# Kernel tuning notes

Measured on AMD Instinct MI355X. Metric: run time of the kernel, lower is better.

## Reference

```python
import math
import jax, jax.numpy as jnp
import numpy as np
from jax import lax

DIM = 4096
N_STEPS = 12 * 4096  # ceil(log2(4096)) * 4096
SEED = 2024


def make_walk_params(seed, n_steps, dim):
    """Deterministic (i, j, cos, sin) schedule for one Kac random walk."""
    key = jax.random.key(seed)
    ki, kj, kt = jax.random.split(key, 3)
    i = jax.random.randint(ki, (n_steps,), 0, dim)
    j = jax.random.randint(kj, (n_steps,), 0, dim - 1)
    j = j + (j >= i).astype(j.dtype)  # ensure j != i
    theta = jax.random.uniform(kt, (n_steps,), minval=0.0, maxval=2.0 * np.pi)
    return (i.astype(jnp.int32), j.astype(jnp.int32),
            jnp.cos(theta).astype(jnp.float32), jnp.sin(theta).astype(jnp.float32))


def kac_walk(x, i_idx, j_idx, cos_t, sin_t):
    """Apply n_steps sequential 2x2 Givens rotations to columns of x [N, dim]."""
    def step(x, p):
        ii, jj, c, s = p
        xi = x[:, ii]
        xj = x[:, jj]
        x = x.at[:, ii].set(c * xi + s * xj)
        x = x.at[:, jj].set(c * xj - s * xi)
        return x, None
    x, _ = lax.scan(step, x, (i_idx, j_idx, cos_t, sin_t))
    return x


def setup_inputs() -> dict:
    key = jax.random.key(0)
    kx, kw, kb, kv = jax.random.split(key, 4)
    x = jax.random.normal(kx, (1, 512, DIM), dtype=jnp.float32)
    W = jax.random.normal(kw, (DIM, DIM), dtype=jnp.float32) / math.sqrt(DIM)
    b = jax.random.normal(kb, (DIM,), dtype=jnp.float32) * 0.01
    vec = jax.random.normal(kv, (DIM,), dtype=jnp.float32) / math.sqrt(DIM)
    i1, j1, c1, s1 = make_walk_params(SEED * 2, N_STEPS, DIM)
    i2, j2, c2, s2 = make_walk_params(SEED * 2 + 1, N_STEPS, DIM)
    return {"x": x, "W": W, "b": b, "vec": vec,
            "i1": i1, "j1": j1, "c1": c1, "s1": s1,
            "i2": i2, "j2": j2, "c2": c2, "s2": s2}


def reference(x, W, b, vec, i1, j1, c1, s1, i2, j2, c2, s2):
    # frozen base layer: y = x @ W.T + b
    y = jnp.einsum('bsd,od->bso', x, W) + b
    # Kac adapter path
    x2d = x.reshape(-1, DIM)                 # [N, dim]
    yp = kac_walk(x2d, i1, j1, c1, s1)
    yp = vec * yp                            # per-coordinate scale
    yp = kac_walk(yp, i2, j2, c2, s2)
    return y + yp.reshape(y.shape)
```

## Files before the change

kernel.cpp:

```cpp
#include <hip/hip_runtime.h>


#define DIM    4096
#define ROWS   512
#define NSTEPS 49152
#define WSTEPS 8192
#define NW2    (NSTEPS / WSTEPS)
#define NSLOT  (2 * NW2)
#define NSG    16
#define CHUNK  128
#define WVN    4
#define PWC    96
#define SLOTREC (WVN * PWC * CHUNK)
#define MAXR   96
#define PADI   4096
#define PADJ   4097
#define KT     1024
#define SPT    (WSTEPS / KT)
#define NCVW   1024
#define NCVX   128

typedef short  short8 __attribute__((ext_vector_type(8)));
typedef __bf16 bf16x8 __attribute__((ext_vector_type(8)));
typedef float  f32x4  __attribute__((ext_vector_type(4)));

__device__ inline short f2bf(float f) {
    unsigned u = __builtin_bit_cast(unsigned, f);
    u += 0x7FFFu + ((u >> 16) & 1u);
    return (short)(u >> 16);
}
__device__ inline short8 pack8(float4 a, float4 b) {
    short8 r;
    r[0] = f2bf(a.x); r[1] = f2bf(a.y); r[2] = f2bf(a.z); r[3] = f2bf(a.w);
    r[4] = f2bf(b.x); r[5] = f2bf(b.y); r[6] = f2bf(b.z); r[7] = f2bf(b.w);
    return r;
}
__device__ inline float bitf(unsigned u) { return __builtin_bit_cast(float, u); }
__device__ inline float2 ldrw(const float2* rw, int boff) {
    return *(const float2*)((const char*)rw + boff);
}
__device__ inline void strw(float2* rw, int boff, float2 v) {
    *(float2*)((char*)rw + boff) = v;
}
__device__ inline void gl16(const short* g, short* l) {
    __builtin_amdgcn_global_load_lds((const __attribute__((address_space(1))) unsigned*)g,
                                     (__attribute__((address_space(3))) unsigned*)l, 16, 0, 0);
}

__global__ __launch_bounds__(KT) void kfused(
    const int* __restrict__ i1, const int* __restrict__ j1,
    const float* __restrict__ c1, const float* __restrict__ s1,
    const int* __restrict__ i2, const int* __restrict__ j2,
    const float* __restrict__ c2, const float* __restrict__ s2,
    uint4* __restrict__ recs, int* __restrict__ nlvls, unsigned* __restrict__ lvmeta_g,
    int doconv, const float* __restrict__ W, const float* __restrict__ X,
    short* __restrict__ wb, short* __restrict__ xb) {

    if (blockIdx.x >= NSLOT) {
        if (!doconv) return;
        const int cb = blockIdx.x - NSLOT;
        const float* src; short* dst; size_t base;
        if (cb < NCVW) { src = W; dst = wb; base = (size_t)cb * 16384; }
        else           { src = X; dst = xb; base = (size_t)(cb - NCVW) * 16384; }
        const size_t o = base + (size_t)threadIdx.x * 16;
        const float4* s4 = (const float4*)(src + o);
        const float4 a0 = s4[0], a1 = s4[1], a2 = s4[2], a3 = s4[3];
        *(short8*)(dst + o)     = pack8(a0, a1);
        *(short8*)(dst + o + 8) = pack8(a2, a3);
        return;
    }

    __shared__ unsigned tbl[DIM];
    __shared__ unsigned spair[WSTEPS];
    __shared__ unsigned lvrk[WSTEPS];
    __shared__ int lcnt[MAXR * NSG];
    __shared__ unsigned lvpk[MAXR], wvbase[MAXR];
    __shared__ unsigned char serf[MAXR];
    __shared__ int nlvlsh;

    const int b    = blockIdx.x;
    const int walk = b / NW2;
    const int w    = b % NW2;
    const int t    = threadIdx.x;
    const int gb   = w * WSTEPS;
    const int sg   = t >> 6;

    const int*   I = walk ? i2 : i1;
    const int*   J = walk ? j2 : j1;
    const float* C = walk ? c2 : c1;
    const float* S = walk ? s2 : s1;

    uint4* slotp = recs + (size_t)b * SLOTREC;

    {
        const uint4 padrec = { (unsigned)(PADI * 8), 0x3F800000u, 0u, (unsigned)(PADJ * 8) };
        for (int k = t; k < SLOTREC; k += KT) slotp[k] = padrec;
    }
    for (int s = t; s < WSTEPS; s += KT)
        spair[s] = (unsigned)I[gb + s] | ((unsigned)J[gb + s] << 16);
    for (int k = t; k < DIM; k += KT) tbl[k] = 0xFFFFFFFFu;
    for (int k = t; k < MAXR * NSG; k += KT) lcnt[k] = 0;
    if (t < MAXR) serf[t] = 0;
    if (t == 0) nlvlsh = 1;
    __syncthreads();

    unsigned pmask = (1u << SPT) - 1u;
    for (int rr = 0; rr < MAXR; ++rr) {
        const unsigned rk = (unsigned)(MAXR - 1 - rr) << 13;
#pragma unroll
        for (int q = 0; q < SPT; ++q)
            if (pmask & (1u << q)) {
                const int s = q * KT + t;
                const unsigned sp = spair[s];
                const unsigned key = rk | (unsigned)s;
                atomicMin(&tbl[sp & 0xFFFFu], key);
                atomicMin(&tbl[sp >> 16], key);
            }
        __syncthreads();
#pragma unroll
        for (int q = 0; q < SPT; ++q)
            if (pmask & (1u << q)) {
                const int s = q * KT + t;
                const unsigned sp = spair[s];
                const unsigned key = rk | (unsigned)s;
                if (tbl[sp & 0xFFFFu] == key && tbl[sp >> 16] == key) {
                    const int rank = atomicAdd(&lcnt[rr * NSG + sg], 1);
                    lvrk[s] = ((unsigned)rank << 8) | (unsigned)rr;
                    pmask &= ~(1u << q);
                }
            }
        const int np = __syncthreads_count(pmask != 0);
        if (np == 0) break;
    }
#pragma unroll
    for (int q = 0; q < SPT; ++q)
        if (pmask & (1u << q)) {
            const int s = q * KT + t;
            const int rank = atomicAdd(&lcnt[(MAXR - 1) * NSG + sg], 1);
            lvrk[s] = ((unsigned)rank << 8) | (unsigned)(MAXR - 1);
        }
    __syncthreads();

    if (t < MAXR) {
        int run = 0;
        for (int g = 0; g < NSG; ++g) {
            const int v = lcnt[t * NSG + g];
            lcnt[t * NSG + g] = run;
            run += v;
        }
        const int nch = (run + 127) >> 7;
        unsigned pk = 0;
        if (run > 0 && nch <= 2) {
            serf[t] = 1;
            pk = (unsigned)nch;
        } else {
#pragma unroll
            for (int wv = 0; wv < WVN; ++wv)
                pk |= (unsigned)((nch + (WVN - 1 - wv)) >> 2) << (8 * wv);
        }
        lvpk[t] = pk;
        if (run > 0) atomicMax(&nlvlsh, t + 1);
    }
    __syncthreads();
    if (t < 64) {
        const int l = t;
        const unsigned w1 = lvpk[l];
        unsigned x1 = w1;
        for (int off = 1; off < 64; off <<= 1) {
            const unsigned v = (unsigned)__shfl_up((int)x1, off);
            if (l >= off) x1 += v;
        }
        wvbase[l] = x1 - w1;
        const unsigned seg1 = (unsigned)__shfl((int)x1, 63);
        const int l2 = 64 + (l & 31);
        const unsigned w2 = lvpk[l2];
        unsigned x2 = w2;
        for (int off = 1; off < 32; off <<= 1) {
            const unsigned v = (unsigned)__shfl_up((int)x2, off);
            if ((l & 31) >= off) x2 += v;
        }
        if (l < 32) wvbase[l2] = seg1 + x2 - w2;
    }
    __syncthreads();
    if (t < MAXR - 1) {
        if (serf[t] && serf[t + 1]) lvpk[t] |= 0x80000000u;
    }
    __syncthreads();
    if (t == 0) nlvls[b] = nlvlsh;
    if (t < MAXR) lvmeta_g[b * MAXR + t] = lvpk[t];

#pragma unroll
    for (int q = 0; q < SPT; ++q) {
        const int s = q * KT + t;
        const unsigned v = lvrk[s];
        const int lvl  = (int)(v & 0xFFu);
        const int rank = (int)(v >> 8) + lcnt[lvl * NSG + sg];
        const int cl   = rank >> 7;
        const int pos  = rank & 127;
        int wv2, wc2;
        if (serf[lvl]) { wv2 = 0; wc2 = cl; }
        else           { wv2 = cl & (WVN - 1); wc2 = cl >> 2; }
        const int pch = (int)((wvbase[lvl] >> (8 * wv2)) & 0xFFu) + wc2;
        if (pch < PWC) {
            const unsigned sp = spair[s];
            const int g = gb + s;
            uint4 r;
            r.x = (sp & 0xFFFFu) * 8u;
            r.y = __builtin_bit_cast(unsigned, C[g]);
            r.z = __builtin_bit_cast(unsigned, S[g]);
            r.w = (sp >> 16) * 8u;
            slotp[((size_t)wv2 * PWC + pch) * CHUNK + pos] = r;
        }
    }
}

__global__ __launch_bounds__(256) void kgemm_bf(const short* __restrict__ Xb, const short* __restrict__ Wb,
                                                const float* __restrict__ bias, float* __restrict__ out,
                                                float* __restrict__ parts, int nks) {
    __shared__ short As[128 * 64];
    __shared__ short Bs[128 * 64];
    const int bid  = blockIdx.x;
    const int ks   = bid % nks;
    const int tile = bid / nks;
    const int bm   = (tile >> 5) * 128;
    const int bn   = (tile & 31) * 128;
    const int tid  = threadIdx.x;
    const int lane = tid & 63;
    const int wv   = tid >> 6;
    const int wr   = (wv >> 1) * 64;
    const int wc   = (wv & 1) * 64;
    const int fr   = lane & 15;
    const int ke   = (lane >> 4) * 8;

    f32x4 acc[4][4];
#pragma unroll
    for (int m = 0; m < 4; ++m)
#pragma unroll
        for (int n = 0; n < 4; ++n) acc[m][n] = (f32x4){0.f, 0.f, 0.f, 0.f};

    const int lrow = lane >> 3;
    const int scol = (((lane & 7) ^ (lrow & 7)) << 3);
    const short* gx = Xb + (size_t)(bm + wv * 32 + lrow) * DIM + scol;
    const short* gw = Wb + (size_t)(bn + wv * 32 + lrow) * DIM + scol;
    short* lA = As + wv * 2048;
    short* lB = Bs + wv * 2048;

    const int nkt   = (DIM / 64) / nks;
    const int kbase = ks * (DIM / nks);
    for (int kt = 0; kt < nkt; ++kt) {
        const int k0 = kbase + kt * 64;
        __syncthreads();
#pragma unroll
        for (int q = 0; q < 4; ++q) {
            gl16(gx + (size_t)(q * 8) * DIM + k0, lA + q * 512);
            gl16(gw + (size_t)(q * 8) * DIM + k0, lB + q * 512);
        }
        __syncthreads();
#pragma unroll
        for (int kk = 0; kk < 64; kk += 32) {
            const int sb = (kk + ke) >> 3;
            short8 af[4], bf[4];
#pragma unroll
            for (int m = 0; m < 4; ++m) {
                const int R = wr + m * 16 + fr;
                af[m] = *(const short8*)&As[R * 64 + ((sb ^ (R & 7)) << 3)];
            }
#pragma unroll
            for (int n = 0; n < 4; ++n) {
                const int R = wc + n * 16 + fr;
                bf[n] = *(const short8*)&Bs[R * 64 + ((sb ^ (R & 7)) << 3)];
            }
#pragma unroll
            for (int m = 0; m < 4; ++m)
#pragma unroll
                for (int n = 0; n < 4; ++n)
                    acc[m][n] = __builtin_amdgcn_mfma_f32_16x16x32_bf16(
                        __builtin_bit_cast(bf16x8, af[m]),
                        __builtin_bit_cast(bf16x8, bf[n]),
                        acc[m][n], 0, 0, 0);
        }
    }
    float* dst = ks ? (parts + (size_t)(ks - 1) * ROWS * DIM) : out;
#pragma unroll
    for (int n = 0; n < 4; ++n) {
        const int col = bn + wc + n * 16 + fr;
        const float bv = ks ? 0.f : bias[col];
#pragma unroll
        for (int m = 0; m < 4; ++m) {
            const int rbase = bm + wr + m * 16 + (lane >> 4) * 4;
#pragma unroll
            for (int r = 0; r < 4; ++r)
                dst[(size_t)(rbase + r) * DIM + col] = acc[m][n][r] + bv;
        }
    }
}

#define LDT 72
__global__ __launch_bounds__(256) void kgemm_small(const float* __restrict__ X, const float* __restrict__ W,
                                                   const float* __restrict__ bias, float* __restrict__ out) {
    __shared__ short As[64 * LDT];
    __shared__ short Bs[128 * LDT];
    const int tid  = threadIdx.x;
    const int bn   = (blockIdx.x & 31) * 128;
    const int bm   = (blockIdx.x >> 5) * 64;
    const int lane = tid & 63;
    const int wv   = tid >> 6;
    const int wr   = (wv >> 1) * 32;
    const int wc   = (wv & 1) * 64;
    const int fr   = lane & 15;
    const int ke   = (lane >> 4) * 8;

    f32x4 acc[2][4];
#pragma unroll
    for (int m = 0; m < 2; ++m)
#pragma unroll
        for (int n = 0; n < 4; ++n) acc[m][n] = (f32x4){0.f, 0.f, 0.f, 0.f};

    const int tr = tid >> 2;
    const int tc = (tid & 3) << 4;

    for (int kt = 0; kt < DIM / 64; ++kt) {
        const int k0 = kt * 64;
        float4 ra[4], rb[2][4];
        {
            const float4* ga = (const float4*)(X + (size_t)(bm + tr) * DIM + k0 + tc);
#pragma unroll
            for (int q = 0; q < 4; ++q) ra[q] = ga[q];
#pragma unroll
            for (int h = 0; h < 2; ++h) {
                const float4* gw = (const float4*)(W + (size_t)(bn + h * 64 + tr) * DIM + k0 + tc);
#pragma unroll
                for (int q = 0; q < 4; ++q) rb[h][q] = gw[q];
            }
        }
        __syncthreads();
        *(short8*)&As[tr * LDT + tc]     = pack8(ra[0], ra[1]);
        *(short8*)&As[tr * LDT + tc + 8] = pack8(ra[2], ra[3]);
#pragma unroll
        for (int h = 0; h < 2; ++h) {
            *(short8*)&Bs[(h * 64 + tr) * LDT + tc]     = pack8(rb[h][0], rb[h][1]);
            *(short8*)&Bs[(h * 64 + tr) * LDT + tc + 8] = pack8(rb[h][2], rb[h][3]);
        }
        __syncthreads();
#pragma unroll
        for (int kk = 0; kk < 64; kk += 32) {
            short8 af[2], bf[4];
#pragma unroll
            for (int m = 0; m < 2; ++m)
                af[m] = *(const short8*)&As[(wr + m * 16 + fr) * LDT + kk + ke];
#pragma unroll
            for (int n = 0; n < 4; ++n)
                bf[n] = *(const short8*)&Bs[(wc + n * 16 + fr) * LDT + kk + ke];
#pragma unroll
            for (int m = 0; m < 2; ++m)
#pragma unroll
                for (int n = 0; n < 4; ++n)
                    acc[m][n] = __builtin_amdgcn_mfma_f32_16x16x32_bf16(
                        __builtin_bit_cast(bf16x8, af[m]),
                        __builtin_bit_cast(bf16x8, bf[n]),
                        acc[m][n], 0, 0, 0);
        }
    }
#pragma unroll
    for (int n = 0; n < 4; ++n) {
        const int col = bn + wc + n * 16 + fr;
        const float bv = bias[col];
#pragma unroll
        for (int m = 0; m < 2; ++m) {
            const int rbase = bm + wr + m * 16 + (lane >> 4) * 4;
#pragma unroll
            for (int r = 0; r < 4; ++r)
                out[(size_t)(rbase + r) * DIM + col] = acc[m][n][r] + bv;
        }
    }
}

__global__ __launch_bounds__(256) void kwalk(const float* __restrict__ X, const float* __restrict__ vec,
                                             const uint4* __restrict__ recs, const int* __restrict__ nlvls,
                                             const unsigned* __restrict__ lvmeta_g,
                                             const float* __restrict__ parts, int nparts,
                                             float* __restrict__ out) {
    __shared__ float2 rw[DIM + 2];
    __shared__ unsigned lvm[MAXR];
    const int tid  = threadIdx.x;
    const int wv   = tid >> 6;
    const int lane = tid & 63;
    const int pr   = blockIdx.x;
    const int rA   = pr * 2, rB = pr * 2 + 1;

    {
        const float4* xa = (const float4*)(X + (size_t)rA * DIM);
        const float4* xb = (const float4*)(X + (size_t)rB * DIM);
        for (int c4 = tid; c4 < DIM / 4; c4 += 256) {
            const float4 a = xa[c4], b = xb[c4];
            rw[c4 * 4 + 0] = make_float2(a.x, b.x);
            rw[c4 * 4 + 1] = make_float2(a.y, b.y);
            rw[c4 * 4 + 2] = make_float2(a.z, b.z);
            rw[c4 * 4 + 3] = make_float2(a.w, b.w);
        }
        if (tid < 2) rw[DIM + tid] = make_float2(0.f, 0.f);
    }

    for (int slot = 0; slot < NSLOT; ++slot) {
        if (slot == NW2) {
            __syncthreads();
            const float4* v4 = (const float4*)vec;
            for (int c4 = tid; c4 < DIM / 4; c4 += 256) {
                const float4 v = v4[c4];
#pragma unroll
                for (int q = 0; q < 4; ++q) {
                    float2 tv = rw[c4 * 4 + q];
                    const float sc = (q == 0) ? v.x : (q == 1) ? v.y : (q == 2) ? v.z : v.w;
                    tv.x *= sc; tv.y *= sc;
                    rw[c4 * 4 + q] = tv;
                }
            }
        }
        if (tid < MAXR) lvm[tid] = lvmeta_g[slot * MAXR + tid];
        const int nlvl = nlvls[slot];
        __syncthreads();

        const uint4* wbase = recs + (size_t)slot * SLOTREC + (size_t)wv * (PWC * CHUNK);
        uint4 r0A = wbase[lane],       r0B = wbase[64 + lane];
        uint4 r1A = wbase[128 + lane], r1B = wbase[192 + lane];
        uint4 r2A = wbase[256 + lane], r2B = wbase[320 + lane];
        int t = 0;

        for (int lvl = 0; lvl < nlvl; ++lvl) {
            const unsigned mm = lvm[lvl];
            int n = (int)((mm >> (wv * 8)) & 0xFFu);
            if (wv == 3) n &= 0x7F;
            for (int it = 0; it < n; ++it) {
                int kc = t + 3; if (kc > PWC - 1) kc = PWC - 1;
                const uint4 mA = wbase[(size_t)kc * CHUNK + lane];
                const uint4 mB = wbase[(size_t)kc * CHUNK + 64 + lane];

                const int   ia = (int)r0A.x, ja = (int)r0A.w;
                const int   ib = (int)r0B.x, jb = (int)r0B.w;
                const float ca = bitf(r0A.y), sa = bitf(r0A.z);
                const float cb = bitf(r0B.y), sb = bitf(r0B.z);
                const float2 gai = ldrw(rw, ia), gaj = ldrw(rw, ja);
                const float2 gbi = ldrw(rw, ib), gbj = ldrw(rw, jb);

                float2 wia, wja, wib, wjb;
                wia.x = fmaf(ca, gai.x,  sa * gaj.x);
                wia.y = fmaf(ca, gai.y,  sa * gaj.y);
                wja.x = fmaf(ca, gaj.x, -sa * gai.x);
                wja.y = fmaf(ca, gaj.y, -sa * gai.y);
                wib.x = fmaf(cb, gbi.x,  sb * gbj.x);
                wib.y = fmaf(cb, gbi.y,  sb * gbj.y);
                wjb.x = fmaf(cb, gbj.x, -sb * gbi.x);
                wjb.y = fmaf(cb, gbj.y, -sb * gbi.y);
                strw(rw, ia, wia); strw(rw, ja, wja);
                strw(rw, ib, wib); strw(rw, jb, wjb);

                r0A = r1A; r0B = r1B;
                r1A = r2A; r1B = r2B;
                r2A = mA;  r2B = mB;
                ++t;
            }
            if (!(mm & 0x80000000u)) {
                __builtin_amdgcn_sched_barrier(0);
                asm volatile("s_waitcnt lgkmcnt(0)" ::: "memory");
                __builtin_amdgcn_s_barrier();
                __builtin_amdgcn_sched_barrier(0);
            }
        }
    }

    float4* oa = (float4*)(out + (size_t)rA * DIM);
    float4* ob = (float4*)(out + (size_t)rB * DIM);
    const size_t PS = (size_t)ROWS * DIM / 4;
    const float4* qa = (const float4*)parts + (size_t)rA * (DIM / 4);
    const float4* qb = (const float4*)parts + (size_t)rB * (DIM / 4);
    for (int c4 = tid; c4 < DIM / 4; c4 += 256) {
        const float2 p0 = rw[c4 * 4 + 0], p1 = rw[c4 * 4 + 1];
        const float2 p2 = rw[c4 * 4 + 2], p3 = rw[c4 * 4 + 3];
        float4 ta = oa[c4], tb = ob[c4];
        for (int p = 0; p < nparts; ++p) {
            const float4 a = qa[c4 + (size_t)p * PS];
            const float4 b = qb[c4 + (size_t)p * PS];
            ta.x += a.x; ta.y += a.y; ta.z += a.z; ta.w += a.w;
            tb.x += b.x; tb.y += b.y; tb.z += b.z; tb.w += b.w;
        }
        ta.x += p0.x; ta.y += p1.x; ta.z += p2.x; ta.w += p3.x;
        tb.x += p0.y; tb.y += p1.y; tb.z += p2.y; tb.w += p3.y;
        oa[c4] = ta; ob[c4] = tb;
    }
}

extern "C" void kernel_launch(void* const* d_in, const int* in_sizes, int n_in,
                              void* d_out, int out_size, void* d_ws, size_t ws_size,
                              hipStream_t stream) {
    const float* X    = (const float*)d_in[0];
    const float* W    = (const float*)d_in[1];
    const float* bias = (const float*)d_in[2];
    const float* vec  = (const float*)d_in[3];
    const int*   i1   = (const int*)d_in[4];
    const int*   j1   = (const int*)d_in[5];
    const float* c1   = (const float*)d_in[6];
    const float* s1   = (const float*)d_in[7];
    const int*   i2   = (const int*)d_in[8];
    const int*   j2   = (const int*)d_in[9];
    const float* c2   = (const float*)d_in[10];
    const float* s2   = (const float*)d_in[11];
    float* out = (float*)d_out;

    const size_t RD         = (size_t)ROWS * DIM * 4;
    const size_t WBB        = (size_t)DIM * DIM * 2;
    const size_t XBB        = (size_t)ROWS * DIM * 2;
    const size_t recs_bytes = (size_t)NSLOT * SLOTREC * 16;
    const size_t off_lvm    = recs_bytes + 1024;
    const size_t off_parts  = recs_bytes + 16384;

    int nks = 0;
    size_t off_wb = 0;
    {
        const size_t need4 = off_parts + 3 * RD + WBB + XBB;
        const size_t need2 = off_parts + 1 * RD + WBB + XBB;
        if      (ws_size >= need4) { nks = 4; off_wb = off_parts + 3 * RD; }
        else if (ws_size >= need2) { nks = 2; off_wb = off_parts + 1 * RD; }
    }

    uint4*    recs   = (uint4*)d_ws;
    int*      nlvlsb = (int*)((char*)d_ws + recs_bytes);
    unsigned* lvmeta = (unsigned*)((char*)d_ws + off_lvm);
    float*    parts  = (float*)((char*)d_ws + off_parts);
    short*    wbuf   = (short*)((char*)d_ws + off_wb);
    short*    xbuf   = (short*)((char*)d_ws + off_wb + WBB);
    const bool bf = (nks > 0);

    hipLaunchKernelGGL(kfused, dim3(NSLOT + (bf ? (NCVW + NCVX) : 0)), dim3(KT), 0, stream,
                       i1, j1, c1, s1, i2, j2, c2, s2, recs, nlvlsb, lvmeta,
                       bf ? 1 : 0, W, X, wbuf, xbuf);
    if (bf)
        hipLaunchKernelGGL(kgemm_bf, dim3(128 * nks), dim3(256), 0, stream,
                           xbuf, wbuf, bias, out, parts, nks);
    else
        hipLaunchKernelGGL(kgemm_small, dim3(256), dim3(256), 0, stream, X, W, bias, out);
    hipLaunchKernelGGL(kwalk, dim3(ROWS / 2), dim3(256), 0, stream,
                       X, vec, recs, nlvlsb, lvmeta, parts, bf ? (nks - 1) : 0, out);
}
```

Baseline: 226.3 us.

## Co-schedule walk and GEMM blocks in one kernel, add final reduction pass

Merges the Kac-walk kernel and the bf16 GEMM kernel into a single launch whose blocks branch on blockIdx, so the latency-bound walk blocks and the MFMA GEMM blocks occupy the GPU at the same time instead of running one after the other. The walk now writes its result to a separate workspace buffer, and a new elementwise kernel sums the GEMM output, the split-K partials and the walk result. The cost is an extra full-size buffer write and read plus one more launch. Walk and GEMM blocks also now share one shared-memory allocation sized for the larger of the two.

```diff
diff --git a/kernel.cpp b/kernel.cpp
--- a/kernel.cpp
+++ b/kernel.cpp
@@ -19,6 +19,7 @@
 #define SPT    (WSTEPS / KT)
 #define NCVW   1024
 #define NCVX   128
+#define SMEMB  33664
 
 typedef short  short8 __attribute__((ext_vector_type(8)));
 typedef __bf16 bf16x8 __attribute__((ext_vector_type(8)));
@@ -91,7 +92,6 @@
     const float* S = walk ? s2 : s1;
 
     uint4* slotp = recs + (size_t)b * SLOTREC;
-
     {
         const uint4 padrec = { (unsigned)(PADI * 8), 0x3F800000u, 0u, (unsigned)(PADJ * 8) };
         for (int k = t; k < SLOTREC; k += KT) slotp[k] = padrec;
@@ -150,10 +150,8 @@
         }
         const int nch = (run + 127) >> 7;
         unsigned pk = 0;
-        if (run > 0 && nch <= 2) {
-            serf[t] = 1;
-            pk = (unsigned)nch;
-        } else {
+        if (run > 0 && nch <= 2) { serf[t] = 1; pk = (unsigned)nch; }
+        else {
 #pragma unroll
             for (int wv = 0; wv < WVN; ++wv)
                 pk |= (unsigned)((nch + (WVN - 1 - wv)) >> 2) << (8 * wv);
@@ -214,12 +212,118 @@
     }
 }
 
-__global__ __launch_bounds__(256) void kgemm_bf(const short* __restrict__ Xb, const short* __restrict__ Wb,
-                                                const float* __restrict__ bias, float* __restrict__ out,
-                                                float* __restrict__ parts, int nks) {
-    __shared__ short As[128 * 64];
-    __shared__ short Bs[128 * 64];
-    const int bid  = blockIdx.x;
+__device__ void walk_body(char* smem, int pr,
+                          const float* __restrict__ X, const float* __restrict__ vec,
+                          const uint4* __restrict__ recs, const int* __restrict__ nlvls,
+                          const unsigned* __restrict__ lvmeta_g,
+                          float* __restrict__ dstbuf, int directadd) {
+    float2* rw = (float2*)smem;
+    unsigned* lvm = (unsigned*)(smem + (DIM + 2) * 8);
+    const int tid  = threadIdx.x;
+    const int wv   = tid >> 6;
+    const int lane = tid & 63;
+    const int rA   = pr * 2, rB = pr * 2 + 1;
+
+    {
+        const float4* xa = (const float4*)(X + (size_t)rA * DIM);
+        const float4* xb = (const float4*)(X + (size_t)rB * DIM);
+        for (int c4 = tid; c4 < DIM / 4; c4 += 256) {
+            const float4 a = xa[c4], b = xb[c4];
+            rw[c4 * 4 + 0] = make_float2(a.x, b.x);
+            rw[c4 * 4 + 1] = make_float2(a.y, b.y);
+            rw[c4 * 4 + 2] = make_float2(a.z, b.z);
+            rw[c4 * 4 + 3] = make_float2(a.w, b.w);
+        }
+        if (tid < 2) rw[DIM + tid] = make_float2(0.f, 0.f);
+    }
+
+    for (int slot = 0; slot < NSLOT; ++slot) {
+        if (slot == NW2) {
+            __syncthreads();
+            const float4* v4 = (const float4*)vec;
+            for (int c4 = tid; c4 < DIM / 4; c4 += 256) {
+                const float4 v = v4[c4];
+#pragma unroll
+                for (int q = 0; q < 4; ++q) {
+                    float2 tv = rw[c4 * 4 + q];
+                    const float sc = (q == 0) ? v.x : (q == 1) ? v.y : (q == 2) ? v.z : v.w;
+                    tv.x *= sc; tv.y *= sc;
+                    rw[c4 * 4 + q] = tv;
+                }
+            }
+        }
+        if (tid < MAXR) lvm[tid] = lvmeta_g[slot * MAXR + tid];
+        const int nlvl = nlvls[slot];
+        __syncthreads();
+
+        const uint4* wbase = recs + (size_t)slot * SLOTREC + (size_t)wv * (PWC * CHUNK);
+        uint4 r0A = wbase[lane],       r0B = wbase[64 + lane];
+        uint4 r1A = wbase[128 + lane], r1B = wbase[192 + lane];
+        uint4 r2A = wbase[256 + lane], r2B = wbase[320 + lane];
+        int t = 0;
+
+        for (int lvl = 0; lvl < nlvl; ++lvl) {
+            const unsigned mm = lvm[lvl];
+            int n = (int)((mm >> (wv * 8)) & 0xFFu);
+            if (wv == 3) n &= 0x7F;
+            for (int it = 0; it < n; ++it) {
+                int kc = t + 3; if (kc > PWC - 1) kc = PWC - 1;
+                const uint4 mA = wbase[(size_t)kc * CHUNK + lane];
+                const uint4 mB = wbase[(size_t)kc * CHUNK + 64 + lane];
+
+                const int   ia = (int)r0A.x, ja = (int)r0A.w;
+                const int   ib = (int)r0B.x, jb = (int)r0B.w;
+                const float ca = bitf(r0A.y), sa = bitf(r0A.z);
+                const float cb = bitf(r0B.y), sb = bitf(r0B.z);
+                const float2 gai = ldrw(rw, ia), gaj = ldrw(rw, ja);
+                const float2 gbi = ldrw(rw, ib), gbj = ldrw(rw, jb);
+
+                float2 wia, wja, wib, wjb;
+                wia.x = fmaf(ca, gai.x,  sa * gaj.x);
+                wia.y = fmaf(ca, gai.y,  sa * gaj.y);
+                wja.x = fmaf(ca, gaj.x, -sa * gai.x);
+                wja.y = fmaf(ca, gaj.y, -sa * gai.y);
+                wib.x = fmaf(cb, gbi.x,  sb * gbj.x);
+                wib.y = fmaf(cb, gbi.y,  sb * gbj.y);
+                wjb.x = fmaf(cb, gbj.x, -sb * gbi.x);
+                wjb.y = fmaf(cb, gbj.y, -sb * gbi.y);
+                strw(rw, ia, wia); strw(rw, ja, wja);
+                strw(rw, ib, wib); strw(rw, jb, wjb);
+
+                r0A = r1A; r0B = r1B;
+                r1A = r2A; r1B = r2B;
+                r2A = mA;  r2B = mB;
+                ++t;
+            }
+            if (!(mm & 0x80000000u)) {
+                __builtin_amdgcn_sched_barrier(0);
+                asm volatile("s_waitcnt lgkmcnt(0)" ::: "memory");
+                __builtin_amdgcn_s_barrier();
+                __builtin_amdgcn_sched_barrier(0);
+            }
+        }
+    }
+
+    float4* oa = (float4*)(dstbuf + (size_t)rA * DIM);
+    float4* ob = (float4*)(dstbuf + (size_t)rB * DIM);
+    for (int c4 = tid; c4 < DIM / 4; c4 += 256) {
+        const float2 p0 = rw[c4 * 4 + 0], p1 = rw[c4 * 4 + 1];
+        const float2 p2 = rw[c4 * 4 + 2], p3 = rw[c4 * 4 + 3];
+        float4 ta, tb;
+        if (directadd) { ta = oa[c4]; tb = ob[c4]; }
+        else           { ta = (float4){0,0,0,0}; tb = (float4){0,0,0,0}; }
+        ta.x += p0.x; ta.y += p1.x; ta.z += p2.x; ta.w += p3.x;
+        tb.x += p0.y; tb.y += p1.y; tb.z += p2.y; tb.w += p3.y;
+        oa[c4] = ta; ob[c4] = tb;
+    }
+}
+
+__device__ void gemm_body(char* smem, int bid,
+                          const short* __restrict__ Xb, const short* __restrict__ Wb,
+                          const float* __restrict__ bias, float* __restrict__ out,
+                          float* __restrict__ parts, int nks) {
+    short* As = (short*)smem;
+    short* Bs = As + 128 * 64;
     const int ks   = bid % nks;
     const int tile = bid / nks;
     const int bm   = (tile >> 5) * 128;
@@ -292,6 +396,40 @@
             for (int r = 0; r < 4; ++r)
                 dst[(size_t)(rbase + r) * DIM + col] = acc[m][n][r] + bv;
         }
+    }
+}
+
+__global__ __launch_bounds__(256) void kboth(
+    const float* __restrict__ X, const float* __restrict__ vec,
+    const uint4* __restrict__ recs, const int* __restrict__ nlvls,
+    const unsigned* __restrict__ lvmeta_g, float* __restrict__ walkbuf,
+    const short* __restrict__ Xb, const short* __restrict__ Wb,
+    const float* __restrict__ bias, float* __restrict__ out,
+    float* __restrict__ parts, int nks) {
+    __shared__ __align__(16) char smem[SMEMB];
+    if (blockIdx.x < ROWS / 2)
+        walk_body(smem, blockIdx.x, X, vec, recs, nlvls, lvmeta_g, walkbuf, 0);
+    else
+        gemm_body(smem, blockIdx.x - ROWS / 2, Xb, Wb, bias, out, parts, nks);
+}
+
+__global__ __launch_bounds__(256) void kadd(float* __restrict__ out,
+                                            const float* __restrict__ walkbuf,
+                                            const float* __restrict__ parts, int nparts) {
+    const size_t N = (size_t)ROWS * DIM / 4;
+    const size_t i0 = (size_t)blockIdx.x * 256 + threadIdx.x;
+    float4* o4 = (float4*)out;
+    const float4* w4 = (const float4*)walkbuf;
+    const float4* p4 = (const float4*)parts;
+    for (size_t i = i0; i < N; i += (size_t)gridDim.x * 256) {
+        float4 t = o4[i];
+        const float4 s = w4[i];
+        t.x += s.x; t.y += s.y; t.z += s.z; t.w += s.w;
+        for (int p = 0; p < nparts; ++p) {
+            const float4 a = p4[i + (size_t)p * N];
+            t.x += a.x; t.y += a.y; t.z += a.z; t.w += a.w;
+        }
+        o4[i] = t;
     }
 }
 
@@ -375,118 +513,12 @@
     }
 }
 
-__global__ __launch_bounds__(256) void kwalk(const float* __restrict__ X, const float* __restrict__ vec,
-                                             const uint4* __restrict__ recs, const int* __restrict__ nlvls,
-                                             const unsigned* __restrict__ lvmeta_g,
-                                             const float* __restrict__ parts, int nparts,
-                                             float* __restrict__ out) {
-    __shared__ float2 rw[DIM + 2];
-    __shared__ unsigned lvm[MAXR];
-    const int tid  = threadIdx.x;
-    const int wv   = tid >> 6;
-    const int lane = tid & 63;
-    const int pr   = blockIdx.x;
-    const int rA   = pr * 2, rB = pr * 2 + 1;
-
-    {
-        const float4* xa = (const float4*)(X + (size_t)rA * DIM);
-        const float4* xb = (const float4*)(X + (size_t)rB * DIM);
-        for (int c4 = tid; c4 < DIM / 4; c4 += 256) {
-            const float4 a = xa[c4], b = xb[c4];
-            rw[c4 * 4 + 0] = make_float2(a.x, b.x);
-            rw[c4 * 4 + 1] = make_float2(a.y, b.y);
-            rw[c4 * 4 + 2] = make_float2(a.z, b.z);
-            rw[c4 * 4 + 3] = make_float2(a.w, b.w);
-        }
-        if (tid < 2) rw[DIM + tid] = make_float2(0.f, 0.f);
-    }
-
-    for (int slot = 0; slot < NSLOT; ++slot) {
-        if (slot == NW2) {
-            __syncthreads();
-            const float4* v4 = (const float4*)vec;
-            for (int c4 = tid; c4 < DIM / 4; c4 += 256) {
-                const float4 v = v4[c4];
-#pragma unroll
-                for (int q = 0; q < 4; ++q) {
-                    float2 tv = rw[c4 * 4 + q];
-                    const float sc = (q == 0) ? v.x : (q == 1) ? v.y : (q == 2) ? v.z : v.w;
-                    tv.x *= sc; tv.y *= sc;
-                    rw[c4 * 4 + q] = tv;
-                }
-            }
-        }
-        if (tid < MAXR) lvm[tid] = lvmeta_g[slot * MAXR + tid];
-        const int nlvl = nlvls[slot];
-        __syncthreads();
-
-        const uint4* wbase = recs + (size_t)slot * SLOTREC + (size_t)wv * (PWC * CHUNK);
-        uint4 r0A = wbase[lane],       r0B = wbase[64 + lane];
-        uint4 r1A = wbase[128 + lane], r1B = wbase[192 + lane];
-        uint4 r2A = wbase[256 + lane], r2B = wbase[320 + lane];
-        int t = 0;
-
-        for (int lvl = 0; lvl < nlvl; ++lvl) {
-            const unsigned mm = lvm[lvl];
-            int n = (int)((mm >> (wv * 8)) & 0xFFu);
-            if (wv == 3) n &= 0x7F;
-            for (int it = 0; it < n; ++it) {
-                int kc = t + 3; if (kc > PWC - 1) kc = PWC - 1;
-                const uint4 mA = wbase[(size_t)kc * CHUNK + lane];
-                const uint4 mB = wbase[(size_t)kc * CHUNK + 64 + lane];
-
-                const int   ia = (int)r0A.x, ja = (int)r0A.w;
-                const int   ib = (int)r0B.x, jb = (int)r0B.w;
-                const float ca = bitf(r0A.y), sa = bitf(r0A.z);
-                const float cb = bitf(r0B.y), sb = bitf(r0B.z);
-                const float2 gai = ldrw(rw, ia), gaj = ldrw(rw, ja);
-                const float2 gbi = ldrw(rw, ib), gbj = ldrw(rw, jb);
-
-                float2 wia, wja, wib, wjb;
-                wia.x = fmaf(ca, gai.x,  sa * gaj.x);
-                wia.y = fmaf(ca, gai.y,  sa * gaj.y);
-                wja.x = fmaf(ca, gaj.x, -sa * gai.x);
-                wja.y = fmaf(ca, gaj.y, -sa * gai.y);
-                wib.x = fmaf(cb, gbi.x,  sb * gbj.x);
-                wib.y = fmaf(cb, gbi.y,  sb * gbj.y);
-                wjb.x = fmaf(cb, gbj.x, -sb * gbi.x);
-                wjb.y = fmaf(cb, gbj.y, -sb * gbi.y);
-                strw(rw, ia, wia); strw(rw, ja, wja);
-                strw(rw, ib, wib); strw(rw, jb, wjb);
-
-                r0A = r1A; r0B = r1B;
-                r1A = r2A; r1B = r2B;
-                r2A = mA;  r2B = mB;
-                ++t;
-            }
-            if (!(mm & 0x80000000u)) {
-                __builtin_amdgcn_sched_barrier(0);
-                asm volatile("s_waitcnt lgkmcnt(0)" ::: "memory");
-                __builtin_amdgcn_s_barrier();
-                __builtin_amdgcn_sched_barrier(0);
-            }
-        }
-    }
-
-    float4* oa = (float4*)(out + (size_t)rA * DIM);
-    float4* ob = (float4*)(out + (size_t)rB * DIM);
-    const size_t PS = (size_t)ROWS * DIM / 4;
-    const float4* qa = (const float4*)parts + (size_t)rA * (DIM / 4);
-    const float4* qb = (const float4*)parts + (size_t)rB * (DIM / 4);
-    for (int c4 = tid; c4 < DIM / 4; c4 += 256) {
-        const float2 p0 = rw[c4 * 4 + 0], p1 = rw[c4 * 4 + 1];
-        const float2 p2 = rw[c4 * 4 + 2], p3 = rw[c4 * 4 + 3];
-        float4 ta = oa[c4], tb = ob[c4];
-        for (int p = 0; p < nparts; ++p) {
-            const float4 a = qa[c4 + (size_t)p * PS];
-            const float4 b = qb[c4 + (size_t)p * PS];
-            ta.x += a.x; ta.y += a.y; ta.z += a.z; ta.w += a.w;
-            tb.x += b.x; tb.y += b.y; tb.z += b.z; tb.w += b.w;
-        }
-        ta.x += p0.x; ta.y += p1.x; ta.z += p2.x; ta.w += p3.x;
-        tb.x += p0.y; tb.y += p1.y; tb.z += p2.y; tb.w += p3.y;
-        oa[c4] = ta; ob[c4] = tb;
-    }
+__global__ __launch_bounds__(256) void kwalk_fb(const float* __restrict__ X, const float* __restrict__ vec,
+                                                const uint4* __restrict__ recs, const int* __restrict__ nlvls,
+                                                const unsigned* __restrict__ lvmeta_g,
+                                                float* __restrict__ out) {
+    __shared__ __align__(16) char smem[SMEMB];
+    walk_body(smem, blockIdx.x, X, vec, recs, nlvls, lvmeta_g, out, 1);
 }
 
 extern "C" void kernel_launch(void* const* d_in, const int* in_sizes, int n_in,
@@ -516,8 +548,8 @@
     int nks = 0;
     size_t off_wb = 0;
     {
-        const size_t need4 = off_parts + 3 * RD + WBB + XBB;
-        const size_t need2 = off_parts + 1 * RD + WBB + XBB;
+        const size_t need4 = off_parts + 3 * RD + WBB + XBB + RD;
+        const size_t need2 = off_parts + 1 * RD + WBB + XBB + RD;
         if      (ws_size >= need4) { nks = 4; off_wb = off_parts + 3 * RD; }
         else if (ws_size >= need2) { nks = 2; off_wb = off_parts + 1 * RD; }
     }
@@ -528,16 +560,21 @@
     float*    parts  = (float*)((char*)d_ws + off_parts);
     short*    wbuf   = (short*)((char*)d_ws + off_wb);
     short*    xbuf   = (short*)((char*)d_ws + off_wb + WBB);
+    float*    wkbuf  = (float*)((char*)d_ws + off_wb + WBB + XBB);
     const bool bf = (nks > 0);
 
     hipLaunchKernelGGL(kfused, dim3(NSLOT + (bf ? (NCVW + NCVX) : 0)), dim3(KT), 0, stream,
                        i1, j1, c1, s1, i2, j2, c2, s2, recs, nlvlsb, lvmeta,
                        bf ? 1 : 0, W, X, wbuf, xbuf);
-    if (bf)
-        hipLaunchKernelGGL(kgemm_bf, dim3(128 * nks), dim3(256), 0, stream,
+    if (bf) {
+        hipLaunchKernelGGL(kboth, dim3(ROWS / 2 + 128 * nks), dim3(256), 0, stream,
+                           X, vec, recs, nlvlsb, lvmeta, wkbuf,
                            xbuf, wbuf, bias, out, parts, nks);
-    else
+        hipLaunchKernelGGL(kadd, dim3(512), dim3(256), 0, stream,
+                           out, wkbuf, parts, nks - 1);
+    } else {
         hipLaunchKernelGGL(kgemm_small, dim3(256), dim3(256), 0, stream, X, W, bias, out);
-    hipLaunchKernelGGL(kwalk, dim3(ROWS / 2), dim3(256), 0, stream,
-                       X, vec, recs, nlvlsb, lvmeta, parts, bf ? (nks - 1) : 0, out);
-}
+        hipLaunchKernelGGL(kwalk_fb, dim3(ROWS / 2), dim3(256), 0, stream,
+                           X, vec, recs, nlvlsb, lvmeta, out);
+    }
+}
```

New measurement: 213.3 us. 1.06x faster.
